# Performance work log

Hardware: AMD Instinct MI355X
Metric: run time of the kernel (lower is better)

## Reference

```python
import jax, jax.numpy as jnp
import numpy as np

B, D, H = 131072, 8, 128


def setup_inputs() -> dict:
    key = jax.random.key(0)
    ks = jax.random.split(key, 8)
    s1 = 1.0 / np.sqrt(D + 1)
    s2 = 1.0 / np.sqrt(H)
    return {
        "z": jax.random.normal(ks[0], (B, D), dtype=jnp.float32),
        "logp_z": jnp.zeros((B, 1), dtype=jnp.float32),
        "t": jax.random.uniform(ks[1], (1,), dtype=jnp.float32),
        "W1": jax.random.normal(ks[2], (D + 1, H), dtype=jnp.float32) * s1,
        "b1": jnp.zeros((H,), dtype=jnp.float32),
        "W2": jax.random.normal(ks[3], (H, H), dtype=jnp.float32) * s2,
        "b2": jnp.zeros((H,), dtype=jnp.float32),
        "W3": jax.random.normal(ks[4], (H, D), dtype=jnp.float32) * s2,
        "b3": jnp.zeros((D,), dtype=jnp.float32),
    }


def _net_single(z_i, t_scalar, W1, b1, W2, b2, W3, b3):
    # z_i: [D] -> dz/dt: [D]; FFJORD-style MLP on concat([z, t])
    x = jnp.concatenate([z_i, t_scalar[None]])  # [D+1]
    h = jnp.tanh(x @ W1 + b1)
    h = jnp.tanh(h @ W2 + b2)
    return h @ W3 + b3


def reference(z, logp_z, t, W1, b1, W2, b2, W3, b3):
    t_scalar = t.reshape(())

    def f_i(z_i):
        return _net_single(z_i, t_scalar, W1, b1, W2, b2, W3, b3)

    # dz/dt for every sample (batched forward)
    dz_dt = jax.vmap(f_i)(z)  # [B, D]
    # Exact Jacobian trace: fused forward-mode batched Jacobian (replaces the
    # original's D sequential autograd.grad reverse-mode calls)
    jac = jax.vmap(jax.jacfwd(f_i))(z)  # [B, D, D]
    trace = jnp.einsum("bii->b", jac)  # [B]
    dlogp_z_dt = -trace[:, None]  # [B, 1]
    return (dz_dt, dlogp_z_dt)
```

## Files before the change

### kernel.cpp

```cpp
#include <hip/hip_runtime.h>
#include <hip/hip_bf16.h>

#define BATCH 131072
#define PITCH_H 72

typedef __bf16 bf16x4 __attribute__((ext_vector_type(4)));
typedef __bf16 bf16x8 __attribute__((ext_vector_type(8)));
typedef float floatx4 __attribute__((ext_vector_type(4)));

#define GLOBAL_AS __attribute__((address_space(1)))
#define LDS_AS __attribute__((address_space(3)))

__device__ __forceinline__ float fast_tanh2(float y) {
    float e = __expf(y);
    return 1.0f - 2.0f * __builtin_amdgcn_rcpf(e + 1.0f);
}


__global__ void prep_kernel(const float* __restrict__ W1,
                            const float* __restrict__ W2,
                            const float* __restrict__ W3,
                            const float* __restrict__ b1,
                            __bf16* __restrict__ ws) {
    int idx = blockIdx.x * 256 + threadIdx.x;
    if (idx < 16384) {
        int j = idx & 7, q = (idx >> 3) & 3, n = (idx >> 5) & 127, kb = idx >> 12;
        int k = kb * 32 + q * 8 + j;
        ws[idx] = (__bf16)(2.0f * W2[k * 128 + n]);
        float c = 0.0f;
        #pragma unroll
        for (int d = 0; d < 8; ++d) c += W3[k * 8 + d] * W1[d * 128 + n];
        ws[16384 + idx] = (__bf16)(W2[n * 128 + k] * c);
    } else if (idx < 20480) {
        int t = idx - 16384;
        int j = t & 7, q = (t >> 3) & 3, n = t >> 5;
        int k = q * 8 + j;
        __bf16 v = (__bf16)0.0f;
        if (k < 9) v = (__bf16)(2.0f * W1[k * 128 + n]);
        else if (k == 9) v = (__bf16)(2.0f * b1[n]);
        else if (k == 10) {
            float b2x = 2.0f * b1[n];
            float hi = (float)(__bf16)b2x;
            v = (__bf16)(b2x - hi);
        }
        ws[32768 + t] = v;
    } else if (idx < 22528) {
        int t = idx - 20480;
        int j = t & 7, q = (t >> 3) & 3, n = (t >> 5) & 15, kb = t >> 9;
        int k = kb * 32 + q * 8 + j;
        ws[36864 + t] = (n < 8) ? (__bf16)W3[k * 8 + n] : (__bf16)0.0f;
    }
}

__global__ __launch_bounds__(256, 2) void cnf_main(
        const float* __restrict__ z, const float* __restrict__ t_ptr,
        const float* __restrict__ b1g, const float* __restrict__ b2g,
        const float* __restrict__ b3g, const __bf16* __restrict__ ws,
        float* __restrict__ out) {
    __shared__ __bf16 sW2s[16384];
    __shared__ __bf16 sGTs[16384];
    __shared__ float sb2f[128];
    __shared__ __align__(16) __bf16 tile[4][16 * PITCH_H];

    const int tid = threadIdx.x;
    const int lane = tid & 63;
    const int w = tid >> 6;
    const int p = lane & 15;
    const int q = lane >> 4;
    const float tval = t_ptr[0];

    const bf16x8* W1g = (const bf16x8*)(ws + 32768);
    const bf16x8* W3g = (const bf16x8*)(ws + 36864);
    bf16x8 w1f[8];
    #pragma unroll
    for (int nt = 0; nt < 8; ++nt) w1f[nt] = W1g[(nt * 16 + p) * 4 + q];
    bf16x8 w3f[4];
    #pragma unroll
    for (int kb = 0; kb < 4; ++kb) w3f[kb] = W3g[(kb * 16 + p) * 4 + q];
    floatx4 b3f = {0.f, 0.f, 0.f, 0.f};
    if (q < 2) b3f = *(const floatx4*)(b3g + q * 4);
    const float b2v = (tid < 128) ? 2.0f * b2g[tid] : 0.0f;

    float4 zc0a, zc1a, zc0b, zc1b;
    {
        const int sb0 = blockIdx.x * 256 + w * 32;
        if (q == 0) {
            const float4* zp0 = (const float4*)(z + (size_t)(sb0 + p) * 8);
            const float4* zp1 = (const float4*)(z + (size_t)(sb0 + 16 + p) * 8);
            zc0a = zp0[0]; zc1a = zp0[1]; zc0b = zp1[0]; zc1b = zp1[1];
        }
    }

    {
        const uint4* srcW2v = (const uint4*)ws;
        const uint4* srcGTv = (const uint4*)(ws + 16384);
        uint4* dstW2v = (uint4*)sW2s;
        uint4* dstGTv = (uint4*)sGTs;
        #pragma unroll
        for (int i = 0; i < 8; ++i) {
            const int idx = tid + i * 256;
            const int wbase = w * 64 + i * 256;
            __builtin_amdgcn_global_load_lds(
                (const GLOBAL_AS uint4*)(srcW2v + idx),
                (LDS_AS uint4*)(dstW2v + wbase), 16, 0, 0);
            __builtin_amdgcn_global_load_lds(
                (const GLOBAL_AS uint4*)(srcGTv + idx),
                (LDS_AS uint4*)(dstGTv + wbase), 16, 0, 0);
        }
    }

    __bf16* T = tile[w];
    const bf16x8* W2sv = (const bf16x8*)sW2s;
    const bf16x8* GTsv = (const bf16x8*)sGTs;

    float4 zn0a, zn1a, zn0b, zn1b;

    #pragma unroll 1
    for (int it = 0; it < 2; ++it) {
        const int sbase = blockIdx.x * 256 + it * 128 + w * 32;

        bf16x8 ax0, ax1;
        #pragma unroll
        for (int j = 0; j < 8; ++j) { ax0[j] = (__bf16)0.0f; ax1[j] = (__bf16)0.0f; }
        if (q == 0) {
            ax0[0] = (__bf16)zc0a.x; ax0[1] = (__bf16)zc0a.y;
            ax0[2] = (__bf16)zc0a.z; ax0[3] = (__bf16)zc0a.w;
            ax0[4] = (__bf16)zc1a.x; ax0[5] = (__bf16)zc1a.y;
            ax0[6] = (__bf16)zc1a.z; ax0[7] = (__bf16)zc1a.w;
            ax1[0] = (__bf16)zc0b.x; ax1[1] = (__bf16)zc0b.y;
            ax1[2] = (__bf16)zc0b.z; ax1[3] = (__bf16)zc0b.w;
            ax1[4] = (__bf16)zc1b.x; ax1[5] = (__bf16)zc1b.y;
            ax1[6] = (__bf16)zc1b.z; ax1[7] = (__bf16)zc1b.w;
        } else if (q == 1) {
            ax0[0] = (__bf16)tval; ax0[1] = (__bf16)1.0f; ax0[2] = (__bf16)1.0f;
            ax1[0] = (__bf16)tval; ax1[1] = (__bf16)1.0f; ax1[2] = (__bf16)1.0f;
        }

        float a1c0[32], a1c1[32];
        bf16x8 aha[4], ahb[4];
        #pragma unroll
        for (int h = 0; h < 2; ++h) {
            floatx4 accA[4], accB[4];
            #pragma unroll
            for (int lt = 0; lt < 4; ++lt) {
                const floatx4 zz = {0.f, 0.f, 0.f, 0.f};
                accA[lt] = __builtin_amdgcn_mfma_f32_16x16x32_bf16(w1f[4 * h + lt], ax0, zz, 0, 0, 0);
                accB[lt] = __builtin_amdgcn_mfma_f32_16x16x32_bf16(w1f[4 * h + lt], ax1, zz, 0, 0, 0);
            }
            #pragma unroll
            for (int lt = 0; lt < 4; ++lt) {
                bf16x4 v;
                #pragma unroll
                for (int r = 0; r < 4; ++r) {
                    const float h1 = fast_tanh2(accA[lt][r]);
                    a1c0[(4 * h + lt) * 4 + r] = __builtin_fmaf(-h1, h1, 1.0f);
                    v[r] = (__bf16)h1;
                }
                *(bf16x4*)&T[p * PITCH_H + lt * 16 + q * 4] = v;
            }
            aha[2 * h]     = *(const bf16x8*)&T[p * PITCH_H + q * 8];
            aha[2 * h + 1] = *(const bf16x8*)&T[p * PITCH_H + 32 + q * 8];
            #pragma unroll
            for (int lt = 0; lt < 4; ++lt) {
                bf16x4 v;
                #pragma unroll
                for (int r = 0; r < 4; ++r) {
                    const float h1 = fast_tanh2(accB[lt][r]);
                    a1c1[(4 * h + lt) * 4 + r] = __builtin_fmaf(-h1, h1, 1.0f);
                    v[r] = (__bf16)h1;
                }
                *(bf16x4*)&T[p * PITCH_H + lt * 16 + q * 4] = v;
            }
            ahb[2 * h]     = *(const bf16x8*)&T[p * PITCH_H + q * 8];
            ahb[2 * h + 1] = *(const bf16x8*)&T[p * PITCH_H + 32 + q * 8];
        }

        if (it == 0) {
            if (q == 0) {
                const int sb1i = blockIdx.x * 256 + 128 + w * 32;
                const float4* zp0 = (const float4*)(z + (size_t)(sb1i + p) * 8);
                const float4* zp1 = (const float4*)(z + (size_t)(sb1i + 16 + p) * 8);
                zn0a = zp0[0]; zn1a = zp0[1]; zn0b = zp1[0]; zn1b = zp1[1];
            }
            if (tid < 128) sb2f[tid] = b2v;
            __syncthreads();
        }

        bf16x8 ah2a[4], ah2b[4];
        #pragma unroll
        for (int h = 0; h < 2; ++h) {
            floatx4 accA[4], accB[4];
            #pragma unroll
            for (int lt = 0; lt < 4; ++lt) {
                const int nt = 4 * h + lt;
                const floatx4 binit = *(const floatx4*)&sb2f[nt * 16 + q * 4];
                floatx4 a = binit, b = binit;
                #pragma unroll
                for (int kb = 0; kb < 4; ++kb) {
                    const bf16x8 wf = W2sv[(kb * 128 + nt * 16 + p) * 4 + q];
                    a = __builtin_amdgcn_mfma_f32_16x16x32_bf16(wf, aha[kb], a, 0, 0, 0);
                    b = __builtin_amdgcn_mfma_f32_16x16x32_bf16(wf, ahb[kb], b, 0, 0, 0);
                }
                accA[lt] = a; accB[lt] = b;
            }
            #pragma unroll
            for (int lt = 0; lt < 4; ++lt) {
                bf16x4 v;
                #pragma unroll
                for (int r = 0; r < 4; ++r) v[r] = (__bf16)fast_tanh2(accA[lt][r]);
                *(bf16x4*)&T[p * PITCH_H + lt * 16 + q * 4] = v;
            }
            ah2a[2 * h]     = *(const bf16x8*)&T[p * PITCH_H + q * 8];
            ah2a[2 * h + 1] = *(const bf16x8*)&T[p * PITCH_H + 32 + q * 8];
            #pragma unroll
            for (int lt = 0; lt < 4; ++lt) {
                bf16x4 v;
                #pragma unroll
                for (int r = 0; r < 4; ++r) v[r] = (__bf16)fast_tanh2(accB[lt][r]);
                *(bf16x4*)&T[p * PITCH_H + lt * 16 + q * 4] = v;
            }
            ah2b[2 * h]     = *(const bf16x8*)&T[p * PITCH_H + q * 8];
            ah2b[2 * h + 1] = *(const bf16x8*)&T[p * PITCH_H + 32 + q * 8];
        }

        floatx4 d3A = b3f, d3B = b3f;
        #pragma unroll
        for (int kb = 0; kb < 4; ++kb) {
            d3A = __builtin_amdgcn_mfma_f32_16x16x32_bf16(w3f[kb], ah2a[kb], d3A, 0, 0, 0);
            d3B = __builtin_amdgcn_mfma_f32_16x16x32_bf16(w3f[kb], ah2b[kb], d3B, 0, 0, 0);
        }
        if (q < 2) {
            *(floatx4*)(out + (size_t)(sbase + p) * 8 + q * 4) = d3A;
            *(floatx4*)(out + (size_t)(sbase + 16 + p) * 8 + q * 4) = d3B;
        }

        bf16x8 aaA[4], aaB[4];
        #pragma unroll
        for (int kb = 0; kb < 4; ++kb) {
            #pragma unroll
            for (int j = 0; j < 8; ++j) {
                const float fa = (float)ah2a[kb][j];
                aaA[kb][j] = (__bf16)__builtin_fmaf(-fa, fa, 1.0f);
                const float fb = (float)ah2b[kb][j];
                aaB[kb][j] = (__bf16)__builtin_fmaf(-fb, fb, 1.0f);
            }
        }

        float trA = 0.f, trB = 0.f;
        #pragma unroll
        for (int nt = 0; nt < 8; ++nt) {
            floatx4 uA = {0.f, 0.f, 0.f, 0.f}, uB = {0.f, 0.f, 0.f, 0.f};
            #pragma unroll
            for (int kb = 0; kb < 4; ++kb) {
                const bf16x8 gf = GTsv[(kb * 128 + nt * 16 + p) * 4 + q];
                uA = __builtin_amdgcn_mfma_f32_16x16x32_bf16(gf, aaA[kb], uA, 0, 0, 0);
                uB = __builtin_amdgcn_mfma_f32_16x16x32_bf16(gf, aaB[kb], uB, 0, 0, 0);
            }
            #pragma unroll
            for (int r = 0; r < 4; ++r) {
                trA = __builtin_fmaf(a1c0[nt * 4 + r], uA[r], trA);
                trB = __builtin_fmaf(a1c1[nt * 4 + r], uB[r], trB);
            }
        }
        trA += __shfl_xor(trA, 16, 64);
        trA += __shfl_xor(trA, 32, 64);
        trB += __shfl_xor(trB, 16, 64);
        trB += __shfl_xor(trB, 32, 64);
        if (lane < 16) {
            out[(size_t)BATCH * 8 + sbase + p] = -trA;
            out[(size_t)BATCH * 8 + sbase + 16 + p] = -trB;
        }

        if (it == 0) { zc0a = zn0a; zc1a = zn1a; zc0b = zn0b; zc1b = zn1b; }
    }
}

extern "C" void kernel_launch(void* const* d_in, const int* in_sizes, int n_in,
                              void* d_out, int out_size, void* d_ws, size_t ws_size,
                              hipStream_t stream) {
    const float* z  = (const float*)d_in[0];
    const float* t  = (const float*)d_in[2];
    const float* W1 = (const float*)d_in[3];
    const float* b1 = (const float*)d_in[4];
    const float* W2 = (const float*)d_in[5];
    const float* b2 = (const float*)d_in[6];
    const float* W3 = (const float*)d_in[7];
    const float* b3 = (const float*)d_in[8];
    __bf16* ws = (__bf16*)d_ws;
    float* out = (float*)d_out;

    prep_kernel<<<88, 256, 0, stream>>>(W1, W2, W3, b1, ws);
    cnf_main<<<512, 256, 0, stream>>>(z, t, b1, b2, b3, ws, out);
}
```

Baseline: 88.74 us.

## Fuse weight preprocessing into main kernel and drop separate prep launch

Removes the prep kernel and has every block of the main kernel build its bf16 weight layouts (scaled W2, W2^T*(W3·W1) trace matrix, W1 and W3 fragments) directly from the fp32 inputs into LDS and registers. This eliminates one kernel launch and the dependency between the two kernels, plus the workspace round trip. The cost is redundant work across 512 blocks: each block recomputes the 128x128 trace-weight product and reads W2 twice from global/L2, which adds ALU and memory traffic before the main compute.

```diff
diff --git a/kernel.cpp b/kernel.cpp
--- a/kernel.cpp
+++ b/kernel.cpp
@@ -7,55 +7,17 @@
 typedef __bf16 bf16x4 __attribute__((ext_vector_type(4)));
 typedef __bf16 bf16x8 __attribute__((ext_vector_type(8)));
 typedef float floatx4 __attribute__((ext_vector_type(4)));
-
-#define GLOBAL_AS __attribute__((address_space(1)))
-#define LDS_AS __attribute__((address_space(3)))
 
 __device__ __forceinline__ float fast_tanh2(float y) {
     float e = __expf(y);
     return 1.0f - 2.0f * __builtin_amdgcn_rcpf(e + 1.0f);
 }
 
-
-__global__ void prep_kernel(const float* __restrict__ W1,
-                            const float* __restrict__ W2,
-                            const float* __restrict__ W3,
-                            const float* __restrict__ b1,
-                            __bf16* __restrict__ ws) {
-    int idx = blockIdx.x * 256 + threadIdx.x;
-    if (idx < 16384) {
-        int j = idx & 7, q = (idx >> 3) & 3, n = (idx >> 5) & 127, kb = idx >> 12;
-        int k = kb * 32 + q * 8 + j;
-        ws[idx] = (__bf16)(2.0f * W2[k * 128 + n]);
-        float c = 0.0f;
-        #pragma unroll
-        for (int d = 0; d < 8; ++d) c += W3[k * 8 + d] * W1[d * 128 + n];
-        ws[16384 + idx] = (__bf16)(W2[n * 128 + k] * c);
-    } else if (idx < 20480) {
-        int t = idx - 16384;
-        int j = t & 7, q = (t >> 3) & 3, n = t >> 5;
-        int k = q * 8 + j;
-        __bf16 v = (__bf16)0.0f;
-        if (k < 9) v = (__bf16)(2.0f * W1[k * 128 + n]);
-        else if (k == 9) v = (__bf16)(2.0f * b1[n]);
-        else if (k == 10) {
-            float b2x = 2.0f * b1[n];
-            float hi = (float)(__bf16)b2x;
-            v = (__bf16)(b2x - hi);
-        }
-        ws[32768 + t] = v;
-    } else if (idx < 22528) {
-        int t = idx - 20480;
-        int j = t & 7, q = (t >> 3) & 3, n = (t >> 5) & 15, kb = t >> 9;
-        int k = kb * 32 + q * 8 + j;
-        ws[36864 + t] = (n < 8) ? (__bf16)W3[k * 8 + n] : (__bf16)0.0f;
-    }
-}
-
 __global__ __launch_bounds__(256, 2) void cnf_main(
         const float* __restrict__ z, const float* __restrict__ t_ptr,
-        const float* __restrict__ b1g, const float* __restrict__ b2g,
-        const float* __restrict__ b3g, const __bf16* __restrict__ ws,
+        const float* __restrict__ W1g, const float* __restrict__ b1g,
+        const float* __restrict__ W2g, const float* __restrict__ b2g,
+        const float* __restrict__ W3g, const float* __restrict__ b3g,
         float* __restrict__ out) {
     __shared__ __bf16 sW2s[16384];
     __shared__ __bf16 sGTs[16384];
@@ -69,17 +31,9 @@
     const int q = lane >> 4;
     const float tval = t_ptr[0];
 
-    const bf16x8* W1g = (const bf16x8*)(ws + 32768);
-    const bf16x8* W3g = (const bf16x8*)(ws + 36864);
-    bf16x8 w1f[8];
-    #pragma unroll
-    for (int nt = 0; nt < 8; ++nt) w1f[nt] = W1g[(nt * 16 + p) * 4 + q];
-    bf16x8 w3f[4];
-    #pragma unroll
-    for (int kb = 0; kb < 4; ++kb) w3f[kb] = W3g[(kb * 16 + p) * 4 + q];
-    floatx4 b3f = {0.f, 0.f, 0.f, 0.f};
-    if (q < 2) b3f = *(const floatx4*)(b3g + q * 4);
-    const float b2v = (tid < 128) ? 2.0f * b2g[tid] : 0.0f;
+    const int tr = tid >> 4, tc = tid & 15;
+    const int k0 = tr * 8, n0 = tc * 8;
+    const int kb_s = tr >> 2, q_s = tr & 3;
 
     float4 zc0a, zc1a, zc0b, zc1b;
     {
@@ -91,21 +45,82 @@
         }
     }
 
+    bf16x8 w1f[8];
+    #pragma unroll
+    for (int nt = 0; nt < 8; ++nt) {
+        const int n = nt * 16 + p;
+        bf16x8 v;
+        #pragma unroll
+        for (int j = 0; j < 8; ++j) v[j] = (__bf16)0.0f;
+        if (q == 0) {
+            #pragma unroll
+            for (int j = 0; j < 8; ++j) v[j] = (__bf16)(2.0f * W1g[j * 128 + n]);
+        } else if (q == 1) {
+            v[0] = (__bf16)(2.0f * W1g[8 * 128 + n]);
+            const float b2x = 2.0f * b1g[n];
+            const float hi = (float)(__bf16)b2x;
+            v[1] = (__bf16)b2x;
+            v[2] = (__bf16)(b2x - hi);
+        }
+        w1f[nt] = v;
+    }
+    bf16x8 w3f[4];
+    #pragma unroll
+    for (int kb = 0; kb < 4; ++kb) {
+        bf16x8 v;
+        #pragma unroll
+        for (int j = 0; j < 8; ++j)
+            v[j] = (p < 8) ? (__bf16)W3g[(kb * 32 + q * 8 + j) * 8 + p] : (__bf16)0.0f;
+        w3f[kb] = v;
+    }
+    floatx4 b3f = {0.f, 0.f, 0.f, 0.f};
+    if (q < 2) b3f = *(const floatx4*)(b3g + q * 4);
+    if (tid < 128) sb2f[tid] = 2.0f * b2g[tid];
+
     {
-        const uint4* srcW2v = (const uint4*)ws;
-        const uint4* srcGTv = (const uint4*)(ws + 16384);
-        uint4* dstW2v = (uint4*)sW2s;
-        uint4* dstGTv = (uint4*)sGTs;
-        #pragma unroll
-        for (int i = 0; i < 8; ++i) {
-            const int idx = tid + i * 256;
-            const int wbase = w * 64 + i * 256;
-            __builtin_amdgcn_global_load_lds(
-                (const GLOBAL_AS uint4*)(srcW2v + idx),
-                (LDS_AS uint4*)(dstW2v + wbase), 16, 0, 0);
-            __builtin_amdgcn_global_load_lds(
-                (const GLOBAL_AS uint4*)(srcGTv + idx),
-                (LDS_AS uint4*)(dstGTv + wbase), 16, 0, 0);
+        float w3blk[8][8];
+        #pragma unroll
+        for (int j = 0; j < 8; ++j) {
+            const float4 a = *(const float4*)(W3g + (k0 + j) * 8);
+            const float4 b = *(const float4*)(W3g + (k0 + j) * 8 + 4);
+            w3blk[j][0] = a.x; w3blk[j][1] = a.y; w3blk[j][2] = a.z; w3blk[j][3] = a.w;
+            w3blk[j][4] = b.x; w3blk[j][5] = b.y; w3blk[j][6] = b.z; w3blk[j][7] = b.w;
+        }
+        #pragma unroll
+        for (int nn = 0; nn < 8; ++nn) {
+            const int n = n0 + nn;
+            float w1c[8];
+            #pragma unroll
+            for (int d = 0; d < 8; ++d) w1c[d] = W1g[d * 128 + n];
+            const float4 g0 = *(const float4*)(W2g + n * 128 + k0);
+            const float4 g1 = *(const float4*)(W2g + n * 128 + k0 + 4);
+            const float w2gt[8] = {g0.x, g0.y, g0.z, g0.w, g1.x, g1.y, g1.z, g1.w};
+            bf16x8 v;
+            #pragma unroll
+            for (int j = 0; j < 8; ++j) {
+                float c = 0.0f;
+                #pragma unroll
+                for (int d = 0; d < 8; ++d) c = __builtin_fmaf(w3blk[j][d], w1c[d], c);
+                v[j] = (__bf16)(w2gt[j] * c);
+            }
+            *(bf16x8*)&sGTs[((kb_s * 128 + n) * 4 + q_s) * 8] = v;
+        }
+    }
+    {
+        float w2blk[8][8];
+        #pragma unroll
+        for (int j = 0; j < 8; ++j) {
+            const float4 a = *(const float4*)(W2g + (k0 + j) * 128 + n0);
+            const float4 b = *(const float4*)(W2g + (k0 + j) * 128 + n0 + 4);
+            w2blk[j][0] = a.x; w2blk[j][1] = a.y; w2blk[j][2] = a.z; w2blk[j][3] = a.w;
+            w2blk[j][4] = b.x; w2blk[j][5] = b.y; w2blk[j][6] = b.z; w2blk[j][7] = b.w;
+        }
+        #pragma unroll
+        for (int nn = 0; nn < 8; ++nn) {
+            bf16x8 v;
+            #pragma unroll
+            for (int j = 0; j < 8; ++j) v[j] = (__bf16)(2.0f * w2blk[j][nn]);
+            *(bf16x8*)&sW2s[((kb_s * 128 + n0 + nn) * 4 + q_s) * 8] = v;
         }
     }
 
@@ -182,7 +197,6 @@
                 const float4* zp1 = (const float4*)(z + (size_t)(sb1i + 16 + p) * 8);
                 zn0a = zp0[0]; zn1a = zp0[1]; zn0b = zp1[0]; zn1b = zp1[1];
             }
-            if (tid < 128) sb2f[tid] = b2v;
             __syncthreads();
         }
 
@@ -286,9 +300,7 @@
     const float* b2 = (const float*)d_in[6];
     const float* W3 = (const float*)d_in[7];
     const float* b3 = (const float*)d_in[8];
-    __bf16* ws = (__bf16*)d_ws;
     float* out = (float*)d_out;
 
-    prep_kernel<<<88, 256, 0, stream>>>(W1, W2, W3, b1, ws);
-    cnf_main<<<512, 256, 0, stream>>>(z, t, b1, b2, b3, ws, out);
+    cnf_main<<<512, 256, 0, stream>>>(z, t, W1, b1, W2, b2, W3, b3, out);
 }
```

After: 101.1 us. 13.9% more time.
